# Kernel tuning notes

Hardware: AMD Instinct MI355X
Metric: run time of the kernel (lower is better)

## Reference

```python
import jax, jax.numpy as jnp
import numpy as np

B, LM, LX, D = 16, 1024, 1024, 768


def setup_inputs() -> dict:
    key = jax.random.key(0)
    k1, k2, k3, k4 = jax.random.split(key, 4)
    main = jax.random.normal(k1, (B, LM, D), dtype=jnp.float32)
    x = jax.random.normal(k2, (B, LX, D), dtype=jnp.float32)
    # keras 'uniform' init ~ U(-0.05, 0.05); scale to keep activations sane
    W = jax.random.uniform(k3, (D, D), dtype=jnp.float32, minval=-0.05, maxval=0.05)
    w = jax.random.uniform(k4, (2 * D, 1), dtype=jnp.float32, minval=-0.05, maxval=0.05)
    return {"main": main, "x": x, "W": W, "w": w}


def reference(main, x, W, w):
    # bilinear co-attention scores: (main @ W) . x^T -> (B, LM, LX)
    proj = jnp.einsum('bmd,de->bme', main, W)            # (B, LM, D)
    scores = jnp.einsum('bme,bne->bmn', proj, x)         # (B, LM, LX) -- no softmax in original
    A = jnp.einsum('bmn,bnd->bmd', scores, x)            # attended features (B, LM, D)
    s = main - A
    m = main * A
    outputs = jnp.concatenate([s, m], axis=-1)           # (B, LM, 2D)
    beta = jnp.einsum('bmk,k->bm', outputs, w[:, 0])     # (B, LM) -- raw, no softmax
    pooled = jnp.einsum('bm,bmk->bk', beta, outputs)     # weighted-sum pooling (B, 2D)
    return pooled
```

## Files before the change

### kernel.cpp

```cpp
#include <hip/hip_runtime.h>

constexpr int kB  = 16;
constexpr int kLM = 1024;
constexpr int kLX = 1024;
constexpr int kD  = 768;

using short8 = __attribute__((ext_vector_type(8))) short;
using f32x4  = __attribute__((ext_vector_type(4))) float;

__device__ __forceinline__ unsigned short f2bf(float f) {
    unsigned u = __float_as_uint(f);
    u = (u + 0x7FFF + ((u >> 16) & 1)) >> 16;
    return (unsigned short)u;
}
__device__ __forceinline__ float bf2f(unsigned short h) {
    return __uint_as_float(((unsigned)h) << 16);
}

__device__ __forceinline__ void gl_lds16(const unsigned short* g, unsigned short* l) {
    auto gp = (const __attribute__((address_space(1))) unsigned int*)g;
    auto lp = (__attribute__((address_space(3))) unsigned int*)l;
    __builtin_amdgcn_global_load_lds(gp, lp, 16, 0, 0);
}

__device__ __forceinline__ void writeChunk(unsigned short* dst, float4 lo, float4 hi) {
    union { short8 v; unsigned short u[8]; } o;
    o.u[0] = f2bf(lo.x); o.u[1] = f2bf(lo.y); o.u[2] = f2bf(lo.z); o.u[3] = f2bf(lo.w);
    o.u[4] = f2bf(hi.x); o.u[5] = f2bf(hi.y); o.u[6] = f2bf(hi.z); o.u[7] = f2bf(hi.w);
    *(short8*)dst = o.v;
}

__device__ __forceinline__ size_t chunk_off(int c, int K) {
    int sr = c >> 3, s = c & 7;
    int tt = s ^ (sr & 7);
    int r  = sr * 2 + (tt >> 2);
    int q  = tt & 3;
    return (size_t)r * K + q * 8;
}

__device__ __forceinline__ void gemm_core(
    const unsigned short* __restrict__ Ab, const unsigned short* __restrict__ Bb,
    unsigned short* __restrict__ Cb, unsigned short* __restrict__ Cm,
    int N, int K, unsigned short* As0, unsigned short* Bs0) {
    const int t    = threadIdx.x;
    const int wave = t >> 6, lane = t & 63;
    const int wr = (wave >> 1) * 64, wc = (wave & 1) * 64;
    const int quad = lane >> 4, l15 = lane & 15;

    const int c0 = t, c1 = t + 256;
    const size_t off0 = chunk_off(c0, K);
    const size_t off1 = chunk_off(c1, K);

    const int sfr  = ((l15 & 1) * 4 + quad) ^ ((l15 >> 1) & 7);
    const int aOff = wr * 32 + (l15 >> 1) * 64 + sfr * 8;
    const int bOff = wc * 32 + (l15 >> 1) * 64 + sfr * 8;

    f32x4 acc[4][4];
    const f32x4 z = {0.f, 0.f, 0.f, 0.f};
#pragma unroll
    for (int i = 0; i < 4; ++i)
#pragma unroll
        for (int j = 0; j < 4; ++j) acc[i][j] = z;

    const int T = K >> 5;

    auto stage = [&](int kt, int sel) {
        const size_t k = (size_t)kt << 5;
        unsigned short* Ad = As0 + sel * 4096;
        unsigned short* Bd = Bs0 + sel * 4096;
        gl_lds16(Ab + off0 + k, Ad + c0 * 8);
        gl_lds16(Ab + off1 + k, Ad + c1 * 8);
        gl_lds16(Bb + off0 + k, Bd + c0 * 8);
        gl_lds16(Bb + off1 + k, Bd + c1 * 8);
    };

    stage(0, 0);
    stage(1, 1);

    for (int kt = 0; kt < T; ++kt) {
        if (kt + 1 < T) asm volatile("s_waitcnt vmcnt(4)" ::: "memory");
        else            asm volatile("s_waitcnt vmcnt(0)" ::: "memory");
        __builtin_amdgcn_s_barrier();
        asm volatile("" ::: "memory");

        const unsigned short* aP = As0 + (kt & 1) * 4096 + aOff;
        const unsigned short* bP = Bs0 + (kt & 1) * 4096 + bOff;
        short8 af[4], bg[4];
#pragma unroll
        for (int i = 0; i < 4; ++i) af[i] = *(const short8*)(aP + i * 512);
#pragma unroll
        for (int j = 0; j < 4; ++j) bg[j] = *(const short8*)(bP + j * 512);
        __builtin_amdgcn_s_setprio(1);
#pragma unroll
        for (int i = 0; i < 4; ++i)
#pragma unroll
            for (int j = 0; j < 4; ++j)
                acc[i][j] = __builtin_amdgcn_mfma_f32_16x16x32_bf16(
                    af[i], bg[j], acc[i][j], 0, 0, 0);
        __builtin_amdgcn_s_setprio(0);
        asm volatile("" ::: "memory");
        __builtin_amdgcn_s_barrier();
        if (kt + 2 < T) stage(kt + 2, kt & 1);
    }

    unsigned short* CbW = Cb + (size_t)wr * N + wc;
#pragma unroll
    for (int i = 0; i < 4; ++i)
#pragma unroll
        for (int j = 0; j < 4; ++j)
#pragma unroll
            for (int r = 0; r < 4; ++r)
                CbW[(size_t)(i * 16 + quad * 4 + r) * N + j * 16 + l15] =
                    f2bf(acc[i][j][r]);

    if (Cm) {
        unsigned short* CmW = Cm + (size_t)wc * N + wr;
#pragma unroll
        for (int i = 0; i < 4; ++i)
#pragma unroll
            for (int j = 0; j < 4; ++j) {
                ushort4 o;
                o.x = f2bf(acc[i][j][0]);
                o.y = f2bf(acc[i][j][1]);
                o.z = f2bf(acc[i][j][2]);
                o.w = f2bf(acc[i][j][3]);
                *(ushort4*)(CmW + (size_t)(j * 16 + l15) * N + i * 16 + quad * 4) = o;
            }
    }
}

__global__ __launch_bounds__(256) void prep_kernel(
    const float* __restrict__ x, unsigned short* __restrict__ xT,
    const float* __restrict__ W, unsigned short* __restrict__ WT,
    const float* __restrict__ mainp, unsigned short* __restrict__ mainBF) {
    const int bid = blockIdx.x;
    const int t   = threadIdx.x;
    if (bid < 3216) {
        __shared__ float tile[64][65];
        const float* src;
        unsigned short* dst;
        int ss, dstride;
        if (bid < 3072) {
            const int lb = bid & 15, rest = bid >> 4;
            const int db = rest % 12, b = rest / 12;
            src = x + ((size_t)b * kLX + lb * 64) * kD + db * 64;
            ss  = kD;
            dst = xT + ((size_t)b * kD + db * 64) * kLX + lb * 64;
            dstride = kLX;
        } else {
            const int ti = bid - 3072;
            const int d0 = (ti / 12) * 64, e0 = (ti % 12) * 64;
            src = W + (size_t)d0 * kD + e0;
            ss  = kD;
            dst = WT + (size_t)e0 * kD + d0;
            dstride = kD;
        }
        const int tx = t & 15, ty = t >> 4;
#pragma unroll
        for (int p = 0; p < 4; ++p) {
            int r = p * 16 + ty;
            float4 v = *(const float4*)(src + (size_t)r * ss + tx * 4);
            *(float4*)&tile[r][tx * 4] = v;
        }
        __syncthreads();
#pragma unroll
        for (int p = 0; p < 4; ++p) {
            int dr = p * 16 + ty;
            ushort4 o;
            o.x = f2bf(tile[tx * 4 + 0][dr]);
            o.y = f2bf(tile[tx * 4 + 1][dr]);
            o.z = f2bf(tile[tx * 4 + 2][dr]);
            o.w = f2bf(tile[tx * 4 + 3][dr]);
            *(ushort4*)(dst + (size_t)dr * dstride + tx * 4) = o;
        }
    } else {
        const long i = (long)(bid - 3216) * 256 + t;
        const long na8 = (long)kB * kLM * kD / 8;
        if (i >= na8) return;
        const float* s = mainp + i * 8;
        writeChunk(mainBF + i * 8, *(const float4*)s, *(const float4*)(s + 4));
    }
}

__global__ __launch_bounds__(256) void gemm_stage2_kernel(
    const unsigned short* __restrict__ xT,
    const unsigned short* __restrict__ mainBF,
    const unsigned short* __restrict__ WT,
    unsigned short* __restrict__ G, unsigned short* __restrict__ P) {
    __shared__ unsigned short As[2][4096];
    __shared__ unsigned short Bs[2][4096];
    const int wgid = blockIdx.x;
    const unsigned short *Ab, *Bb;
    unsigned short *Cb, *Cm = nullptr;
    int K;
    if (wgid < 336) {
        const int xcd = wgid & 7, kk = wgid >> 3;
        const int grp = kk / 21, til = kk - grp * 21;
        const int b   = grp * 8 + xcd;
        int bi = (int)((sqrtf(8.f * (float)til + 1.f) - 1.f) * 0.5f);
        if (bi * (bi + 1) / 2 > til) --bi;
        else if ((bi + 1) * (bi + 2) / 2 <= til) ++bi;
        const int bj = til - bi * (bi + 1) / 2;
        K = kLX;
        const unsigned short* base = xT + (size_t)b * kD * kLX;
        Ab = base + (size_t)bi * 128 * kLX;
        Bb = base + (size_t)bj * 128 * kLX;
        unsigned short* Gb = G + (size_t)b * kD * kD;
        Cb = Gb + (size_t)bi * 128 * kD + bj * 128;
        if (bi != bj) Cm = Gb + (size_t)bj * 128 * kD + bi * 128;
    } else {
        const int pid = wgid - 336;
        const int xcd = pid & 7, kk = pid >> 3;
        const int grp = kk / 48, til = kk - grp * 48;
        const int b   = grp * 8 + xcd;
        const int bi  = til & 7, bj = til >> 3;
        K = kD;
        Ab = mainBF + (size_t)b * kLM * kD + (size_t)bi * 128 * kD;
        Bb = WT + (size_t)bj * 128 * kD;
        Cb = P + (size_t)b * kLM * kD + (size_t)bi * 128 * kD + bj * 128;
    }
    gemm_core(Ab, Bb, Cb, Cm, kD, K, &As[0][0], &Bs[0][0]);
}

__global__ __launch_bounds__(256) void gemm_a_kernel(
    const unsigned short* __restrict__ P, const unsigned short* __restrict__ G,
    unsigned short* __restrict__ Ao) {
    __shared__ unsigned short As[2][4096];
    __shared__ unsigned short Bs[2][4096];
    const int wgid = blockIdx.x;
    const int xcd = wgid & 7, kk = wgid >> 3;
    const int grp = kk / 48, til = kk - grp * 48;
    const int b   = grp * 8 + xcd;
    const int bi  = til & 7, bj = til >> 3;
    const unsigned short* Ab = P + (size_t)b * kLM * kD + (size_t)bi * 128 * kD;
    const unsigned short* Bb = G + (size_t)b * kD * kD + (size_t)bj * 128 * kD;
    unsigned short* Cb = Ao + (size_t)b * kLM * kD + (size_t)bi * 128 * kD + bj * 128;
    gemm_core(Ab, Bb, Cb, nullptr, kD, kD, &As[0][0], &Bs[0][0]);
}

__global__ __launch_bounds__(256) void pool_kernel(
    const float* __restrict__ mainp, const unsigned short* __restrict__ Aout,
    const float* __restrict__ w, float* __restrict__ out) {
    __shared__ float red[4][24][64];
    const int b     = blockIdx.y;
    const int chunk = blockIdx.x;
    const int t     = threadIdx.x;
    const int wave  = t >> 6, lane = t & 63;
    float w1[12], w2[12], ps[12], pm[12];
#pragma unroll
    for (int s = 0; s < 12; ++s) {
        w1[s] = w[s * 64 + lane];
        w2[s] = w[kD + s * 64 + lane];
        ps[s] = 0.f; pm[s] = 0.f;
    }
#pragma unroll
    for (int rr = 0; rr < 4; ++rr) {
        const int row = chunk * 16 + rr * 4 + wave;
        const float* mr = mainp + ((size_t)b * kLM + row) * kD;
        const unsigned short* ar = Aout + ((size_t)b * kLM + row) * kD;
        float sv[12], mv[12], acc = 0.f;
#pragma unroll
        for (int s = 0; s < 12; ++s) {
            float m_ = mr[s * 64 + lane];
            float a_ = bf2f(ar[s * 64 + lane]);
            sv[s] = m_ - a_;
            mv[s] = m_ * a_;
            acc += sv[s] * w1[s] + mv[s] * w2[s];
        }
#pragma unroll
        for (int off = 32; off; off >>= 1) acc += __shfl_xor(acc, off);
#pragma unroll
        for (int s = 0; s < 12; ++s) { ps[s] += acc * sv[s]; pm[s] += acc * mv[s]; }
    }
#pragma unroll
    for (int s = 0; s < 12; ++s) {
        red[wave][s][lane]      = ps[s];
        red[wave][12 + s][lane] = pm[s];
    }
    __syncthreads();
    float* ob = out + (size_t)b * 2 * kD;
    for (int v = t; v < 24 * 64; v += 256) {
        const int sl = v >> 6, ln = v & 63;
        const float sum = red[0][sl][ln] + red[1][sl][ln] +
                          red[2][sl][ln] + red[3][sl][ln];
        const int d = (sl < 12) ? sl * 64 + ln : kD + (sl - 12) * 64 + ln;
        atomicAdd(&ob[d], sum);
    }
}

extern "C" void kernel_launch(void* const* d_in, const int* in_sizes, int n_in,
                              void* d_out, int out_size, void* d_ws, size_t ws_size,
                              hipStream_t stream) {
    const float* mainp = (const float*)d_in[0];
    const float* x     = (const float*)d_in[1];
    const float* W     = (const float*)d_in[2];
    const float* w     = (const float*)d_in[3];
    float* out = (float*)d_out;

    char* p = (char*)d_ws;
    unsigned short* xT     = (unsigned short*)p; p += (size_t)kB * kD * kLX * 2;
    unsigned short* G      = (unsigned short*)p; p += (size_t)kB * kD * kD * 2;
    unsigned short* P      = (unsigned short*)p; p += (size_t)kB * kLM * kD * 2;
    unsigned short* Ao     = (unsigned short*)p; p += (size_t)kB * kLM * kD * 2;
    unsigned short* WT     = (unsigned short*)p; p += (size_t)kD * kD * 2;
    unsigned short* mainBF = (unsigned short*)p; p += (size_t)kB * kLM * kD * 2;

    hipMemsetAsync(out, 0, (size_t)kB * 2 * kD * sizeof(float), stream);

    prep_kernel<<<dim3(3216 + kB * kLM * kD / 8 / 256), 256, 0, stream>>>(
        x, xT, W, WT, mainp, mainBF);

    gemm_stage2_kernel<<<dim3(336 + 768), 256, 0, stream>>>(xT, mainBF, WT, G, P);

    gemm_a_kernel<<<dim3(768), 256, 0, stream>>>(P, G, Ao);

    pool_kernel<<<dim3(kLM / 16, kB), 256, 0, stream>>>(mainp, Ao, w, out);
}
```

Baseline: 231.7 us.

## Double GEMM K-tile depth to 64 with new swizzled LDS layout

Each GEMM main-loop step now covers K=64 instead of 32. Every thread issues four 16-byte global-to-LDS loads per operand, and the LDS swizzle is rewritten so each row holds 64 contiguous bf16 elements with an XOR chunk permutation. Each stage performs two MFMA sub-steps, which halves the number of barriers and waitcnt stalls per unit of work. LDS use per block doubles to 64 KB, which can reduce how many blocks fit on each CU.

```diff
diff --git a/kernel.cpp b/kernel.cpp
--- a/kernel.cpp
+++ b/kernel.cpp
@@ -28,14 +28,6 @@
     o.u[0] = f2bf(lo.x); o.u[1] = f2bf(lo.y); o.u[2] = f2bf(lo.z); o.u[3] = f2bf(lo.w);
     o.u[4] = f2bf(hi.x); o.u[5] = f2bf(hi.y); o.u[6] = f2bf(hi.z); o.u[7] = f2bf(hi.w);
     *(short8*)dst = o.v;
-}
-
-__device__ __forceinline__ size_t chunk_off(int c, int K) {
-    int sr = c >> 3, s = c & 7;
-    int tt = s ^ (sr & 7);
-    int r  = sr * 2 + (tt >> 2);
-    int q  = tt & 3;
-    return (size_t)r * K + q * 8;
 }
 
 __device__ __forceinline__ void gemm_core(
@@ -47,13 +39,20 @@
     const int wr = (wave >> 1) * 64, wc = (wave & 1) * 64;
     const int quad = lane >> 4, l15 = lane & 15;
 
-    const int c0 = t, c1 = t + 256;
-    const size_t off0 = chunk_off(c0, K);
-    const size_t off1 = chunk_off(c1, K);
-
-    const int sfr  = ((l15 & 1) * 4 + quad) ^ ((l15 >> 1) & 7);
-    const int aOff = wr * 32 + (l15 >> 1) * 64 + sfr * 8;
-    const int bOff = wc * 32 + (l15 >> 1) * 64 + sfr * 8;
+    size_t goff[4];
+    int    lof[4];
+#pragma unroll
+    for (int m = 0; m < 4; ++m) {
+        const int p   = t + 256 * m;
+        const int row = p >> 3;
+        const int ch  = (p & 7) ^ (row & 7);
+        goff[m] = (size_t)row * K + ch * 8;
+        lof[m]  = p * 8;
+    }
+
+    const int perm0 = quad ^ (l15 & 7);
+    const int aOff  = (wr + l15) * 64 + perm0 * 8;
+    const int bOff  = (wc + l15) * 64 + perm0 * 8;
 
     f32x4 acc[4][4];
     const f32x4 z = {0.f, 0.f, 0.f, 0.f};
@@ -62,41 +61,53 @@
 #pragma unroll
         for (int j = 0; j < 4; ++j) acc[i][j] = z;
 
-    const int T = K >> 5;
+    const int T = K >> 6;
 
     auto stage = [&](int kt, int sel) {
-        const size_t k = (size_t)kt << 5;
-        unsigned short* Ad = As0 + sel * 4096;
-        unsigned short* Bd = Bs0 + sel * 4096;
-        gl_lds16(Ab + off0 + k, Ad + c0 * 8);
-        gl_lds16(Ab + off1 + k, Ad + c1 * 8);
-        gl_lds16(Bb + off0 + k, Bd + c0 * 8);
-        gl_lds16(Bb + off1 + k, Bd + c1 * 8);
+        const size_t k = (size_t)kt << 6;
+        unsigned short* Ad = As0 + sel * 8192;
+        unsigned short* Bd = Bs0 + sel * 8192;
+#pragma unroll
+        for (int m = 0; m < 4; ++m) gl_lds16(Ab + goff[m] + k, Ad + lof[m]);
+#pragma unroll
+        for (int m = 0; m < 4; ++m) gl_lds16(Bb + goff[m] + k, Bd + lof[m]);
     };
 
     stage(0, 0);
     stage(1, 1);
 
     for (int kt = 0; kt < T; ++kt) {
-        if (kt + 1 < T) asm volatile("s_waitcnt vmcnt(4)" ::: "memory");
+        if (kt + 1 < T) asm volatile("s_waitcnt vmcnt(8)" ::: "memory");
         else            asm volatile("s_waitcnt vmcnt(0)" ::: "memory");
         __builtin_amdgcn_s_barrier();
         asm volatile("" ::: "memory");
 
-        const unsigned short* aP = As0 + (kt & 1) * 4096 + aOff;
-        const unsigned short* bP = Bs0 + (kt & 1) * 4096 + bOff;
-        short8 af[4], bg[4];
-#pragma unroll
-        for (int i = 0; i < 4; ++i) af[i] = *(const short8*)(aP + i * 512);
-#pragma unroll
-        for (int j = 0; j < 4; ++j) bg[j] = *(const short8*)(bP + j * 512);
+        const unsigned short* aP = As0 + (kt & 1) * 8192;
+        const unsigned short* bP = Bs0 + (kt & 1) * 8192;
+        short8 a0[4], b0[4], a1[4], b1[4];
+#pragma unroll
+        for (int i = 0; i < 4; ++i) a0[i] = *(const short8*)(aP + aOff + i * 1024);
+#pragma unroll
+        for (int j = 0; j < 4; ++j) b0[j] = *(const short8*)(bP + bOff + j * 1024);
         __builtin_amdgcn_s_setprio(1);
 #pragma unroll
         for (int i = 0; i < 4; ++i)
 #pragma unroll
             for (int j = 0; j < 4; ++j)
                 acc[i][j] = __builtin_amdgcn_mfma_f32_16x16x32_bf16(
-                    af[i], bg[j], acc[i][j], 0, 0, 0);
+                    a0[i], b0[j], acc[i][j], 0, 0, 0);
+        __builtin_amdgcn_s_setprio(0);
+#pragma unroll
+        for (int i = 0; i < 4; ++i) a1[i] = *(const short8*)(aP + (aOff ^ 32) + i * 1024);
+#pragma unroll
+        for (int j = 0; j < 4; ++j) b1[j] = *(const short8*)(bP + (bOff ^ 32) + j * 1024);
+        __builtin_amdgcn_s_setprio(1);
+#pragma unroll
+        for (int i = 0; i < 4; ++i)
+#pragma unroll
+            for (int j = 0; j < 4; ++j)
+                acc[i][j] = __builtin_amdgcn_mfma_f32_16x16x32_bf16(
+                    a1[i], b1[j], acc[i][j], 0, 0, 0);
         __builtin_amdgcn_s_setprio(0);
         asm volatile("" ::: "memory");
         __builtin_amdgcn_s_barrier();
@@ -187,8 +198,8 @@
     const unsigned short* __restrict__ mainBF,
     const unsigned short* __restrict__ WT,
     unsigned short* __restrict__ G, unsigned short* __restrict__ P) {
-    __shared__ unsigned short As[2][4096];
-    __shared__ unsigned short Bs[2][4096];
+    __shared__ unsigned short As[2][8192];
+    __shared__ unsigned short Bs[2][8192];
     const int wgid = blockIdx.x;
     const unsigned short *Ab, *Bb;
     unsigned short *Cb, *Cm = nullptr;
@@ -225,8 +236,8 @@
 __global__ __launch_bounds__(256) void gemm_a_kernel(
     const unsigned short* __restrict__ P, const unsigned short* __restrict__ G,
     unsigned short* __restrict__ Ao) {
-    __shared__ unsigned short As[2][4096];
-    __shared__ unsigned short Bs[2][4096];
+    __shared__ unsigned short As[2][8192];
+    __shared__ unsigned short Bs[2][8192];
     const int wgid = blockIdx.x;
     const int xcd = wgid & 7, kk = wgid >> 3;
     const int grp = kk / 48, til = kk - grp * 48;
```

Result: faster. 216.2 us (-6.7%).
